# Kernel optimization log

Hardware: AMD Instinct MI355X
Metric: run time of the kernel (lower is better)

Reference implementation:

```python
import jax, jax.numpy as jnp
import numpy as np

B = 65536  # batch size


def setup_inputs() -> dict:
    key = jax.random.key(0)
    ks = jax.random.split(key, 8)
    x = jax.random.normal(ks[0], (B, 784), dtype=jnp.float32)
    conv_w = jax.random.normal(ks[1], (3, 3), dtype=jnp.float32)
    w1 = jax.random.normal(ks[2], (676, 256), dtype=jnp.float32) * 0.04
    b1 = jnp.zeros((256,), dtype=jnp.float32)
    w2 = jax.random.normal(ks[3], (256, 128), dtype=jnp.float32) * 0.06
    b2 = jnp.zeros((128,), dtype=jnp.float32)
    w3 = jax.random.normal(ks[4], (128, 10), dtype=jnp.float32) * 0.09
    b3 = jnp.zeros((10,), dtype=jnp.float32)
    return {"x": x, "conv_w": conv_w, "w1": w1, "b1": b1,
            "w2": w2, "b2": b2, "w3": w3, "b3": b3}


def reference(x, conv_w, w1, b1, w2, b2, w3, b3):
    # x: [B, 784] -> images [B, 1, 28, 28]
    img = x.reshape(-1, 1, 28, 28)
    # Convolve() is a valid cross-correlation (tensordot of window with kernel,
    # no flip) -> lax.conv_general_dilated (also no kernel flip).
    kern = conv_w.reshape(1, 1, 3, 3)  # [O, I, kh, kw]
    y = jax.lax.conv_general_dilated(
        img, kern, window_strides=(1, 1), padding="VALID",
        dimension_numbers=("NCHW", "OIHW", "NCHW"))  # [B, 1, 26, 26]
    h = y.reshape(y.shape[0], 26 * 26)
    h = jax.nn.relu(h @ w1 + b1)
    h = jax.nn.relu(h @ w2 + b2)
    return h @ w3 + b3  # [B, 10] logits
```

## Files before the change

kernel.cpp:

```cpp
#include <hip/hip_runtime.h>
#include <hip/hip_bf16.h>

typedef __bf16 bf16x8 __attribute__((ext_vector_type(8)));
typedef float  f32x4  __attribute__((ext_vector_type(4)));

#define B_ROWS 65536
#define MR 32
#define H0S 712
#define H1S 264
#define H2S 136
#define KC1 22
#define KC2 8
#define KC3 4

#define W1B_ELEMS (704*256)
#define W2B_ELEMS (256*128)
#define W3B_ELEMS (128*16)

__global__ void pack_weights(const float* __restrict__ w1,
                             const float* __restrict__ w2,
                             const float* __restrict__ w3,
                             __hip_bfloat16* __restrict__ w1b,
                             __hip_bfloat16* __restrict__ w2b,
                             __hip_bfloat16* __restrict__ w3b) {
    int idx = blockIdx.x * 256 + threadIdx.x;
    if (idx < W1B_ELEMS) {
        int ki = idx & 31, t = idx >> 5;
        int n = t & 255, kc = t >> 8;
        int k = kc * 32 + ki;
        float v = (k < 676) ? w1[k * 256 + n] : 0.0f;
        w1b[idx] = __float2bfloat16(v);
    } else if (idx < W1B_ELEMS + W2B_ELEMS) {
        int j = idx - W1B_ELEMS;
        int ki = j & 31, t = j >> 5;
        int n = t & 127, kc = t >> 7;
        w2b[j] = __float2bfloat16(w2[(kc * 32 + ki) * 128 + n]);
    } else if (idx < W1B_ELEMS + W2B_ELEMS + W3B_ELEMS) {
        int j = idx - W1B_ELEMS - W2B_ELEMS;
        int ki = j & 31, t = j >> 5;
        int n = t & 15, kc = t >> 4;
        float v = (n < 10) ? w3[(kc * 32 + ki) * 10 + n] : 0.0f;
        w3b[j] = __float2bfloat16(v);
    }
}

__global__ __launch_bounds__(256, 2)
void fused_model(const float* __restrict__ x, const float* __restrict__ cw,
                 const __hip_bfloat16* __restrict__ w1b, const float* __restrict__ b1,
                 const __hip_bfloat16* __restrict__ w2b, const float* __restrict__ b2,
                 const __hip_bfloat16* __restrict__ w3b, const float* __restrict__ b3,
                 float* __restrict__ out) {
    __shared__ __align__(16) char smem[MR * H0S * 2 + MR * H1S * 2];
    __hip_bfloat16* h0s = (__hip_bfloat16*)smem;
    __hip_bfloat16* h1s = (__hip_bfloat16*)(smem + MR * H0S * 2);
    __hip_bfloat16* h2s = (__hip_bfloat16*)smem;

    const int tid = threadIdx.x;
    const int r0  = blockIdx.x * MR;

    const float c00 = cw[0], c01 = cw[1], c02 = cw[2];
    const float c10 = cw[3], c11 = cw[4], c12 = cw[5];
    const float c20 = cw[6], c21 = cw[7], c22 = cw[8];

    for (int t = tid; t < MR * 26; t += 256) {
        int r = t / 26;
        int i = t - r * 26;
        const float* xr = x + (size_t)(r0 + r) * 784 + i * 28;
        float acc[26];
        #pragma unroll
        for (int j = 0; j < 26; j++) acc[j] = 0.0f;
        #pragma unroll
        for (int di = 0; di < 3; di++) {
            float rb[28];
            const float4* p4 = (const float4*)(xr + di * 28);
            #pragma unroll
            for (int q = 0; q < 7; q++) {
                float4 v = p4[q];
                rb[q*4+0] = v.x; rb[q*4+1] = v.y; rb[q*4+2] = v.z; rb[q*4+3] = v.w;
            }
            const float k0 = (di == 0) ? c00 : ((di == 1) ? c10 : c20);
            const float k1 = (di == 0) ? c01 : ((di == 1) ? c11 : c21);
            const float k2 = (di == 0) ? c02 : ((di == 1) ? c12 : c22);
            #pragma unroll
            for (int j = 0; j < 26; j++)
                acc[j] += k0 * rb[j] + k1 * rb[j+1] + k2 * rb[j+2];
        }
        __hip_bfloat16* hp = h0s + r * H0S + i * 26;
        #pragma unroll
        for (int j = 0; j < 26; j++) hp[j] = __float2bfloat16(acc[j]);
    }
    for (int t = tid; t < MR * 36; t += 256) {
        int r = t / 36;
        int c = 676 + (t - r * 36);
        h0s[r * H0S + c] = __float2bfloat16(0.0f);
    }
    __syncthreads();

    const int wave = tid >> 6;
    const int lane = tid & 63;
    const int l15  = lane & 15;
    const int g    = lane >> 4;

    {
        f32x4 acc[2][4];
        #pragma unroll
        for (int mt = 0; mt < 2; mt++)
            #pragma unroll
            for (int nt = 0; nt < 4; nt++)
                acc[mt][nt] = (f32x4){0.f, 0.f, 0.f, 0.f};
        const int nb = wave * 64;
        for (int kc = 0; kc < KC1; kc++) {
            bf16x8 a[2], b[4];
            #pragma unroll
            for (int mt = 0; mt < 2; mt++)
                a[mt] = *(const bf16x8*)(h0s + (mt * 16 + l15) * H0S + kc * 32 + g * 8);
            #pragma unroll
            for (int nt = 0; nt < 4; nt++)
                b[nt] = *(const bf16x8*)(w1b + ((kc * 256 + nb + nt * 16 + l15) * 32 + g * 8));
            #pragma unroll
            for (int mt = 0; mt < 2; mt++)
                #pragma unroll
                for (int nt = 0; nt < 4; nt++)
                    acc[mt][nt] = __builtin_amdgcn_mfma_f32_16x16x32_bf16(
                        a[mt], b[nt], acc[mt][nt], 0, 0, 0);
        }
        #pragma unroll
        for (int nt = 0; nt < 4; nt++) {
            const int n = nb + nt * 16 + l15;
            const float bias = b1[n];
            #pragma unroll
            for (int mt = 0; mt < 2; mt++) {
                #pragma unroll
                for (int q = 0; q < 4; q++) {
                    const int row = mt * 16 + g * 4 + q;
                    float v = acc[mt][nt][q] + bias;
                    h1s[row * H1S + n] = __float2bfloat16(fmaxf(v, 0.0f));
                }
            }
        }
    }
    __syncthreads();

    {
        f32x4 acc[2][2];
        #pragma unroll
        for (int mt = 0; mt < 2; mt++)
            #pragma unroll
            for (int nt = 0; nt < 2; nt++)
                acc[mt][nt] = (f32x4){0.f, 0.f, 0.f, 0.f};
        const int nb = wave * 32;
        for (int kc = 0; kc < KC2; kc++) {
            bf16x8 a[2], b[2];
            #pragma unroll
            for (int mt = 0; mt < 2; mt++)
                a[mt] = *(const bf16x8*)(h1s + (mt * 16 + l15) * H1S + kc * 32 + g * 8);
            #pragma unroll
            for (int nt = 0; nt < 2; nt++)
                b[nt] = *(const bf16x8*)(w2b + ((kc * 128 + nb + nt * 16 + l15) * 32 + g * 8));
            #pragma unroll
            for (int mt = 0; mt < 2; mt++)
                #pragma unroll
                for (int nt = 0; nt < 2; nt++)
                    acc[mt][nt] = __builtin_amdgcn_mfma_f32_16x16x32_bf16(
                        a[mt], b[nt], acc[mt][nt], 0, 0, 0);
        }
        #pragma unroll
        for (int nt = 0; nt < 2; nt++) {
            const int n = nb + nt * 16 + l15;
            const float bias = b2[n];
            #pragma unroll
            for (int mt = 0; mt < 2; mt++) {
                #pragma unroll
                for (int q = 0; q < 4; q++) {
                    const int row = mt * 16 + g * 4 + q;
                    float v = acc[mt][nt][q] + bias;
                    h2s[row * H2S + n] = __float2bfloat16(fmaxf(v, 0.0f));
                }
            }
        }
    }
    __syncthreads();

    if (wave < 2) {
        f32x4 acc3 = (f32x4){0.f, 0.f, 0.f, 0.f};
        for (int kc = 0; kc < KC3; kc++) {
            bf16x8 a = *(const bf16x8*)(h2s + (wave * 16 + l15) * H2S + kc * 32 + g * 8);
            bf16x8 b = *(const bf16x8*)(w3b + ((kc * 16 + l15) * 32 + g * 8));
            acc3 = __builtin_amdgcn_mfma_f32_16x16x32_bf16(a, b, acc3, 0, 0, 0);
        }
        if (l15 < 10) {
            const float bias = b3[l15];
            #pragma unroll
            for (int q = 0; q < 4; q++) {
                const int row = wave * 16 + g * 4 + q;
                out[(size_t)(r0 + row) * 10 + l15] = acc3[q] + bias;
            }
        }
    }
}

extern "C" void kernel_launch(void* const* d_in, const int* in_sizes, int n_in,
                              void* d_out, int out_size, void* d_ws, size_t ws_size,
                              hipStream_t stream) {
    const float* x  = (const float*)d_in[0];
    const float* cw = (const float*)d_in[1];
    const float* w1 = (const float*)d_in[2];
    const float* b1 = (const float*)d_in[3];
    const float* w2 = (const float*)d_in[4];
    const float* b2 = (const float*)d_in[5];
    const float* w3 = (const float*)d_in[6];
    const float* b3 = (const float*)d_in[7];
    float* out = (float*)d_out;

    __hip_bfloat16* w1b = (__hip_bfloat16*)d_ws;
    __hip_bfloat16* w2b = w1b + W1B_ELEMS;
    __hip_bfloat16* w3b = w2b + W2B_ELEMS;

    const int pack_total = W1B_ELEMS + W2B_ELEMS + W3B_ELEMS;
    pack_weights<<<(pack_total + 255) / 256, 256, 0, stream>>>(w1, w2, w3, w1b, w2b, w3b);
    fused_model<<<B_ROWS / MR, 256, 0, stream>>>(x, cw, w1b, b1, w2b, b2, w3b, b3, out);
}
```

Measured before the change: 360.6 us.

## Fold the convolution into W1 and stream x directly into the first GEMM

Because the 3x3 convolution and the first dense layer are both linear, the pack kernel now builds an effective 784x256 bf16 weight matrix, W1e = conv^T · W1. The main kernel reads raw x rows from global memory, converts them to bf16 in registers and feeds them straight into the MFMA loop. This removes the per-block convolution pass, the large shared-memory h0 staging buffer and one barrier. The first-layer loop also prefetches the next A/B fragments into registers, and the lower shared-memory footprint allows a launch bound of 4 blocks per CU. In exchange, the K dimension grows from 704 to 800, x is loaded redundantly by all four waves (relying on cache), and applying the conv in bf16 weights slightly changes the rounding.

```diff
diff --git a/kernel.cpp b/kernel.cpp
--- a/kernel.cpp
+++ b/kernel.cpp
@@ -5,38 +5,51 @@
 typedef float  f32x4  __attribute__((ext_vector_type(4)));
 
 #define B_ROWS 65536
-#define MR 32
-#define H0S 712
+#define KC1 25
+#define KC2 8
+#define KC3 4
 #define H1S 264
 #define H2S 136
-#define KC1 22
-#define KC2 8
-#define KC3 4
-
-#define W1B_ELEMS (704*256)
+
+#define W1E_ELEMS (800*256)
 #define W2B_ELEMS (256*128)
 #define W3B_ELEMS (128*16)
 
-__global__ void pack_weights(const float* __restrict__ w1,
+__global__ void pack_weights(const float* __restrict__ cw,
+                             const float* __restrict__ w1,
                              const float* __restrict__ w2,
                              const float* __restrict__ w3,
-                             __hip_bfloat16* __restrict__ w1b,
+                             __hip_bfloat16* __restrict__ w1e,
                              __hip_bfloat16* __restrict__ w2b,
                              __hip_bfloat16* __restrict__ w3b) {
     int idx = blockIdx.x * 256 + threadIdx.x;
-    if (idx < W1B_ELEMS) {
+    if (idx < W1E_ELEMS) {
         int ki = idx & 31, t = idx >> 5;
         int n = t & 255, kc = t >> 8;
         int k = kc * 32 + ki;
-        float v = (k < 676) ? w1[k * 256 + n] : 0.0f;
-        w1b[idx] = __float2bfloat16(v);
-    } else if (idx < W1B_ELEMS + W2B_ELEMS) {
-        int j = idx - W1B_ELEMS;
+        float acc = 0.0f;
+        if (k < 784) {
+            int pi = k / 28, pj = k - pi * 28;
+            #pragma unroll
+            for (int di = 0; di < 3; di++) {
+                int i = pi - di;
+                if (i < 0 || i >= 26) continue;
+                #pragma unroll
+                for (int dj = 0; dj < 3; dj++) {
+                    int j = pj - dj;
+                    if (j < 0 || j >= 26) continue;
+                    acc += cw[di * 3 + dj] * w1[(i * 26 + j) * 256 + n];
+                }
+            }
+        }
+        w1e[idx] = __float2bfloat16(acc);
+    } else if (idx < W1E_ELEMS + W2B_ELEMS) {
+        int j = idx - W1E_ELEMS;
         int ki = j & 31, t = j >> 5;
         int n = t & 127, kc = t >> 7;
         w2b[j] = __float2bfloat16(w2[(kc * 32 + ki) * 128 + n]);
-    } else if (idx < W1B_ELEMS + W2B_ELEMS + W3B_ELEMS) {
-        int j = idx - W1B_ELEMS - W2B_ELEMS;
+    } else if (idx < W1E_ELEMS + W2B_ELEMS + W3B_ELEMS) {
+        int j = idx - W1E_ELEMS - W2B_ELEMS;
         int ki = j & 31, t = j >> 5;
         int n = t & 15, kc = t >> 4;
         float v = (n < 10) ? w3[(kc * 32 + ki) * 10 + n] : 0.0f;
@@ -44,85 +57,84 @@
     }
 }
 
-__global__ __launch_bounds__(256, 2)
-void fused_model(const float* __restrict__ x, const float* __restrict__ cw,
-                 const __hip_bfloat16* __restrict__ w1b, const float* __restrict__ b1,
-                 const __hip_bfloat16* __restrict__ w2b, const float* __restrict__ b2,
-                 const __hip_bfloat16* __restrict__ w3b, const float* __restrict__ b3,
-                 float* __restrict__ out) {
-    __shared__ __align__(16) char smem[MR * H0S * 2 + MR * H1S * 2];
-    __hip_bfloat16* h0s = (__hip_bfloat16*)smem;
-    __hip_bfloat16* h1s = (__hip_bfloat16*)(smem + MR * H0S * 2);
-    __hip_bfloat16* h2s = (__hip_bfloat16*)smem;
-
-    const int tid = threadIdx.x;
-    const int r0  = blockIdx.x * MR;
-
-    const float c00 = cw[0], c01 = cw[1], c02 = cw[2];
-    const float c10 = cw[3], c11 = cw[4], c12 = cw[5];
-    const float c20 = cw[6], c21 = cw[7], c22 = cw[8];
-
-    for (int t = tid; t < MR * 26; t += 256) {
-        int r = t / 26;
-        int i = t - r * 26;
-        const float* xr = x + (size_t)(r0 + r) * 784 + i * 28;
-        float acc[26];
-        #pragma unroll
-        for (int j = 0; j < 26; j++) acc[j] = 0.0f;
-        #pragma unroll
-        for (int di = 0; di < 3; di++) {
-            float rb[28];
-            const float4* p4 = (const float4*)(xr + di * 28);
-            #pragma unroll
-            for (int q = 0; q < 7; q++) {
-                float4 v = p4[q];
-                rb[q*4+0] = v.x; rb[q*4+1] = v.y; rb[q*4+2] = v.z; rb[q*4+3] = v.w;
-            }
-            const float k0 = (di == 0) ? c00 : ((di == 1) ? c10 : c20);
-            const float k1 = (di == 0) ? c01 : ((di == 1) ? c11 : c21);
-            const float k2 = (di == 0) ? c02 : ((di == 1) ? c12 : c22);
-            #pragma unroll
-            for (int j = 0; j < 26; j++)
-                acc[j] += k0 * rb[j] + k1 * rb[j+1] + k2 * rb[j+2];
-        }
-        __hip_bfloat16* hp = h0s + r * H0S + i * 26;
-        #pragma unroll
-        for (int j = 0; j < 26; j++) hp[j] = __float2bfloat16(acc[j]);
-    }
-    for (int t = tid; t < MR * 36; t += 256) {
-        int r = t / 36;
-        int c = 676 + (t - r * 36);
-        h0s[r * H0S + c] = __float2bfloat16(0.0f);
-    }
-    __syncthreads();
-
+__device__ __forceinline__ bf16x8 cvt8(float4 u0, float4 u1) {
+    bf16x8 a;
+    a[0] = (__bf16)u0.x; a[1] = (__bf16)u0.y; a[2] = (__bf16)u0.z; a[3] = (__bf16)u0.w;
+    a[4] = (__bf16)u1.x; a[5] = (__bf16)u1.y; a[6] = (__bf16)u1.z; a[7] = (__bf16)u1.w;
+    return a;
+}
+
+__global__ __launch_bounds__(256, 4)
+void model_kernel(const float* __restrict__ x,
+                  const __hip_bfloat16* __restrict__ w1e, const float* __restrict__ b1,
+                  const __hip_bfloat16* __restrict__ w2b, const float* __restrict__ b2,
+                  const __hip_bfloat16* __restrict__ w3b, const float* __restrict__ b3,
+                  float* __restrict__ out) {
+    __shared__ __align__(16) __hip_bfloat16 h1s[32 * H1S];
+    __shared__ __align__(16) __hip_bfloat16 h2s[32 * H2S];
+
+    const int tid  = threadIdx.x;
     const int wave = tid >> 6;
     const int lane = tid & 63;
     const int l15  = lane & 15;
     const int g    = lane >> 4;
+    const int r0   = blockIdx.x * 32;
 
     {
+        const float* a0p = x + (size_t)(r0 + l15) * 784;
+        const float* a1p = x + (size_t)(r0 + 16 + l15) * 784;
+        const int nb = wave * 64;
+        const __hip_bfloat16* bbase = w1e + ((size_t)(nb + l15) * 32 + g * 8);
+
         f32x4 acc[2][4];
         #pragma unroll
         for (int mt = 0; mt < 2; mt++)
             #pragma unroll
             for (int nt = 0; nt < 4; nt++)
                 acc[mt][nt] = (f32x4){0.f, 0.f, 0.f, 0.f};
-        const int nb = wave * 64;
+
+        int col0 = g * 8;
+        bf16x8 bcur[4], acur[2];
+        {
+            float4 u0 = *(const float4*)(a0p + col0);
+            float4 u1 = *(const float4*)(a0p + col0 + 4);
+            float4 v0 = *(const float4*)(a1p + col0);
+            float4 v1 = *(const float4*)(a1p + col0 + 4);
+            acur[0] = cvt8(u0, u1);
+            acur[1] = cvt8(v0, v1);
+        }
+        #pragma unroll
+        for (int nt = 0; nt < 4; nt++)
+            bcur[nt] = *(const bf16x8*)(bbase + nt * 512);
+
         for (int kc = 0; kc < KC1; kc++) {
-            bf16x8 a[2], b[4];
-            #pragma unroll
-            for (int mt = 0; mt < 2; mt++)
-                a[mt] = *(const bf16x8*)(h0s + (mt * 16 + l15) * H0S + kc * 32 + g * 8);
-            #pragma unroll
-            for (int nt = 0; nt < 4; nt++)
-                b[nt] = *(const bf16x8*)(w1b + ((kc * 256 + nb + nt * 16 + l15) * 32 + g * 8));
+            bf16x8 bnext[4], anext[2];
+            if (kc + 1 < KC1) {
+                int col = (kc + 1) * 32 + g * 8;
+                if (col > 776) col = 776;
+                float4 u0 = *(const float4*)(a0p + col);
+                float4 u1 = *(const float4*)(a0p + col + 4);
+                float4 v0 = *(const float4*)(a1p + col);
+                float4 v1 = *(const float4*)(a1p + col + 4);
+                const __hip_bfloat16* bp = bbase + (size_t)(kc + 1) * 8192;
+                #pragma unroll
+                for (int nt = 0; nt < 4; nt++)
+                    bnext[nt] = *(const bf16x8*)(bp + nt * 512);
+                anext[0] = cvt8(u0, u1);
+                anext[1] = cvt8(v0, v1);
+            }
             #pragma unroll
             for (int mt = 0; mt < 2; mt++)
                 #pragma unroll
                 for (int nt = 0; nt < 4; nt++)
                     acc[mt][nt] = __builtin_amdgcn_mfma_f32_16x16x32_bf16(
-                        a[mt], b[nt], acc[mt][nt], 0, 0, 0);
+                        acur[mt], bcur[nt], acc[mt][nt], 0, 0, 0);
+            if (kc + 1 < KC1) {
+                #pragma unroll
+                for (int nt = 0; nt < 4; nt++) bcur[nt] = bnext[nt];
+                acur[0] = anext[0];
+                acur[1] = anext[1];
+            }
         }
         #pragma unroll
         for (int nt = 0; nt < 4; nt++) {
@@ -149,6 +161,7 @@
             for (int nt = 0; nt < 2; nt++)
                 acc[mt][nt] = (f32x4){0.f, 0.f, 0.f, 0.f};
         const int nb = wave * 32;
+        #pragma unroll
         for (int kc = 0; kc < KC2; kc++) {
             bf16x8 a[2], b[2];
             #pragma unroll
@@ -156,7 +169,7 @@
                 a[mt] = *(const bf16x8*)(h1s + (mt * 16 + l15) * H1S + kc * 32 + g * 8);
             #pragma unroll
             for (int nt = 0; nt < 2; nt++)
-                b[nt] = *(const bf16x8*)(w2b + ((kc * 128 + nb + nt * 16 + l15) * 32 + g * 8));
+                b[nt] = *(const bf16x8*)(w2b + (((size_t)kc * 128 + nb + nt * 16 + l15) * 32 + g * 8));
             #pragma unroll
             for (int mt = 0; mt < 2; mt++)
                 #pragma unroll
@@ -183,9 +196,10 @@
 
     if (wave < 2) {
         f32x4 acc3 = (f32x4){0.f, 0.f, 0.f, 0.f};
+        #pragma unroll
         for (int kc = 0; kc < KC3; kc++) {
             bf16x8 a = *(const bf16x8*)(h2s + (wave * 16 + l15) * H2S + kc * 32 + g * 8);
-            bf16x8 b = *(const bf16x8*)(w3b + ((kc * 16 + l15) * 32 + g * 8));
+            bf16x8 b = *(const bf16x8*)(w3b + (((size_t)kc * 16 + l15) * 32 + g * 8));
             acc3 = __builtin_amdgcn_mfma_f32_16x16x32_bf16(a, b, acc3, 0, 0, 0);
         }
         if (l15 < 10) {
@@ -212,11 +226,11 @@
     const float* b3 = (const float*)d_in[7];
     float* out = (float*)d_out;
 
-    __hip_bfloat16* w1b = (__hip_bfloat16*)d_ws;
-    __hip_bfloat16* w2b = w1b + W1B_ELEMS;
+    __hip_bfloat16* w1e = (__hip_bfloat16*)d_ws;
+    __hip_bfloat16* w2b = w1e + W1E_ELEMS;
     __hip_bfloat16* w3b = w2b + W2B_ELEMS;
 
-    const int pack_total = W1B_ELEMS + W2B_ELEMS + W3B_ELEMS;
-    pack_weights<<<(pack_total + 255) / 256, 256, 0, stream>>>(w1, w2, w3, w1b, w2b, w3b);
-    fused_model<<<B_ROWS / MR, 256, 0, stream>>>(x, cw, w1b, b1, w2b, b2, w3b, b3, out);
-}
+    const int pack_total = W1E_ELEMS + W2B_ELEMS + W3B_ELEMS;
+    pack_weights<<<(pack_total + 255) / 256, 256, 0, stream>>>(cw, w1, w2, w3, w1e, w2b, w3b);
+    model_kernel<<<B_ROWS / 32, 256, 0, stream>>>(x, w1e, b1, w2b, b2, w3b, b3, out);
+}
```

Result: slower. 389.0 us (+7.9%).
